# Kernel tuning notes

Measured on AMD Instinct MI355X. Metric: run time of the kernel, lower is better.

The kernel has to match this reference:

```python
import jax, jax.numpy as jnp
import numpy as np

LENA, BATCH, ARR, HID = 8, 128, 1024, 64


def setup_inputs() -> dict:
    key = jax.random.key(0)
    ks = jax.random.split(key, 7)
    s = 0.1  # keep gates out of saturation
    return {
        "x": jax.random.normal(ks[0], (BATCH, ARR, 1), jnp.float32),
        "hn": jnp.zeros((LENA, BATCH, HID), jnp.float32),  # per-LSTM h0 (torch (1,B,H) squeezed)
        "Wih": jax.random.normal(ks[1], (LENA, 4 * HID, 1), jnp.float32) * s,
        "Whh": jax.random.normal(ks[2], (LENA, 4 * HID, HID), jnp.float32) * s,
        "bih": jax.random.normal(ks[3], (LENA, 4 * HID), jnp.float32) * s,
        "bhh": jax.random.normal(ks[4], (LENA, 4 * HID), jnp.float32) * s,
        "Wl": jax.random.normal(ks[5], (LENA, ARR), jnp.float32) * s,
        "bl": jax.random.normal(ks[6], (LENA,), jnp.float32) * s,
    }


def _ensemble_lstm_last_unit(x, hn, Wih, Whh, bias):
    # x: (B, T); hn: (L, B, H). All L LSTMs run fused in one scan over time.
    L, B, H = hn.shape
    c0 = jnp.zeros_like(hn)

    def step(carry, x_t):  # x_t: (B,)
        h, c = carry  # (L, B, H)
        gates = (x_t[None, :, None] * Wih[:, None, :, 0]
                 + jnp.einsum('lbh,lgh->lbg', h, Whh)
                 + bias[:, None, :])  # (L, B, 4H)
        i, f, g, o = jnp.split(gates, 4, axis=-1)  # torch gate order i,f,g,o
        i, f, o = jax.nn.sigmoid(i), jax.nn.sigmoid(f), jax.nn.sigmoid(o)
        c = f * c + i * jnp.tanh(g)
        h = o * jnp.tanh(c)
        return (h, c), h[:, :, -1]  # emit last hidden unit: o[:, :, -1]

    _, ys = jax.lax.scan(step, (hn, c0), x.T)  # ys: (T, L, B)
    return ys


def reference(x, hn, Wih, Whh, bih, bhh, Wl, bl):
    bias = bih + bhh  # (L, 4H)
    ys = _ensemble_lstm_last_unit(x[:, :, 0], hn, Wih, Whh, bias)  # (T, L, B)
    r = ys.sum(axis=1).T  # sum over ensemble -> (B, T=arr_size)
    return r @ Wl.T + bl  # (B, lenA)
```

## Files before the change

kernel.cpp:

```cpp
#include <hip/hip_runtime.h>


#define LENA 8
#define NB 128
#define NT 1024
#define NH 64

typedef __attribute__((ext_vector_type(4))) float f32x4;
typedef __attribute__((ext_vector_type(8))) short bf16x8;

__device__ __forceinline__ short f2bf(float f) {
    unsigned u = __float_as_uint(f);
    unsigned r = (u + 0x7FFFu + ((u >> 16) & 1u)) >> 16;
    return (short)r;
}

__global__ __launch_bounds__(256, 2) void lstm_v16_kernel(
    const float* __restrict__ x, const float* __restrict__ hn,
    const float* __restrict__ Wih, const float* __restrict__ Whh,
    const float* __restrict__ bih, const float* __restrict__ bhh,
    const float* __restrict__ Wl, float* __restrict__ ws)
{
    __shared__ float x2[NT][2];
    __shared__ float ring[NT][2];
    __shared__ __align__(16) short hbuf[2][16][8];
    __shared__ float pws[2][2][8];

    const int tid = threadIdx.x;
    const int w   = tid >> 6;
    const int l   = tid & 63;
    const int col = l & 15;
    const int kg  = l >> 4;
    const int bb  = kg & 1;
    const int li  = blockIdx.x >> 6;
    const int bg  = blockIdx.x & 63;
    const int b0  = bg * 2;

    for (int i = tid; i < 2 * NT; i += 256) {
        int bx = i >> 10, t = i & (NT - 1);
        x2[t][bx] = x[(size_t)(b0 + bx) * NT + t];
    }
    if (tid < 128) {
        int b = tid >> 6, u = tid & 63;
        float v = hn[((size_t)li * NB + b0 + b) * NH + u];
        int slot = b * 8 + ((u >> 3) ^ (2 * b));
        hbuf[0][slot][u & 7] = f2bf(v);
    }

    const float RLN2 = 1.44269504f;
    bf16x8 bf[4][2];
    #pragma unroll
    for (int g = 0; g < 4; ++g) {
        const float sc = (g == 2) ? 2.0f * RLN2 : RLN2;
        const float* rp = Whh + ((size_t)li * 256 + 64 * g + 16 * w + col) * 64 + kg * 8;
        #pragma unroll
        for (int kh = 0; kh < 2; ++kh) {
            const float* q = rp + kh * 32;
            bf16x8 f;
            #pragma unroll
            for (int e = 0; e < 8; ++e) f[e] = f2bf(sc * q[e]);
            bf[g][kh] = f;
        }
    }
    const int u_c = 16 * w + col;
    float wih4[4];
    f32x4 cinit[4];
    #pragma unroll
    for (int g = 0; g < 4; ++g) {
        const float sc = (g == 2) ? 2.0f * RLN2 : RLN2;
        int rowc = li * 256 + 64 * g + u_c;
        wih4[g] = sc * Wih[rowc];
        float bv = sc * (bih[rowc] + bhh[rowc]);
        cinit[g][0] = bv; cinit[g][1] = bv; cinit[g][2] = bv; cinit[g][3] = bv;
    }

    const int b_r = (col >> 2) & 1;
    const int s0 = b_r * 8 + (kg ^ (2 * b_r));
    const int s1 = b_r * 8 + ((4 + kg) ^ (2 * b_r));
    const int wslot = bb * 8 + ((u_c >> 3) ^ (2 * bb));
    const int wpos  = u_c & 7;
    const bool isring = (u_c == 63);

    float cst = 0.0f;

    __syncthreads();

    #pragma unroll 2
    for (int t = 0; t < NT; ++t) {
        const int p = t & 1;
        bf16x8 a0 = *(const bf16x8*)&hbuf[p][s0][0];
        bf16x8 a1 = *(const bf16x8*)&hbuf[p][s1][0];
        const float xv = x2[t][bb];

        f32x4 acc[4];
        __builtin_amdgcn_s_setprio(1);
        #pragma unroll
        for (int g = 0; g < 4; ++g) {
            f32x4 a = __builtin_amdgcn_mfma_f32_16x16x32_bf16(a0, bf[g][0], cinit[g], 0, 0, 0);
            acc[g] = __builtin_amdgcn_mfma_f32_16x16x32_bf16(a1, bf[g][1], a, 0, 0, 0);
        }
        __builtin_amdgcn_s_setprio(0);
        __builtin_amdgcn_sched_barrier(0);

        float gi = fmaf(xv, wih4[0], acc[0][0]);
        float gf = fmaf(xv, wih4[1], acc[1][0]);
        float gg = fmaf(xv, wih4[2], acc[2][0]);
        float go = fmaf(xv, wih4[3], acc[3][0]);

        float iv = __builtin_amdgcn_rcpf(1.0f + __builtin_amdgcn_exp2f(-gi));
        float fv = __builtin_amdgcn_rcpf(1.0f + __builtin_amdgcn_exp2f(-gf));
        float gt = fmaf(-5.77078016f, __builtin_amdgcn_rcpf(1.0f + __builtin_amdgcn_exp2f(gg)), 2.88539008f);
        float ov = __builtin_amdgcn_rcpf(1.0f + __builtin_amdgcn_exp2f(-go));
        cst = fmaf(fv, cst, iv * gt);
        float ct = fmaf(-2.0f, __builtin_amdgcn_rcpf(1.0f + __builtin_amdgcn_exp2f(cst)), 1.0f);
        float hh = ov * ct;

        unsigned pk;
        asm("v_cvt_pk_bf16_f32 %0, %1, %2" : "=v"(pk) : "v"(hh), "v"(hh));
        hbuf[p ^ 1][wslot][wpos] = (short)(pk & 0xffffu);
        if (isring) ring[t][bb] = hh;
        __syncthreads();
    }

    {
        const int b = w >> 1, p2 = w & 1;
        const int a = l & 7, ch = l >> 3;
        const int tb = p2 * 512 + ch * 64;
        const float* wlp = Wl + (size_t)a * NT + tb;
        float pacc = 0.0f;
        #pragma unroll 4
        for (int i = 0; i < 64; ++i)
            pacc = fmaf(ring[tb + i][b], wlp[i], pacc);
        pacc += __shfl_xor(pacc, 8);
        pacc += __shfl_xor(pacc, 16);
        pacc += __shfl_xor(pacc, 32);
        if (l < 8) pws[b][p2][a] = pacc;
    }
    __syncthreads();
    if (tid < 16) {
        int b = tid >> 3, a = tid & 7;
        ws[((size_t)blockIdx.x * 2 + b) * 8 + a] = pws[b][0][a] + pws[b][1][a];
    }
}

__global__ __launch_bounds__(256) void reduce_kernel(
    const float* __restrict__ ws, const float* __restrict__ bl, float* __restrict__ out)
{
    int tid = blockIdx.x * 256 + threadIdx.x;
    if (tid >= NB * LENA) return;
    int b = tid >> 3, a = tid & 7;
    int bg = b >> 1, bx = b & 1;
    float s = bl[a];
    #pragma unroll
    for (int li = 0; li < LENA; ++li)
        s += ws[(((size_t)li * 64 + bg) * 2 + bx) * 8 + a];
    out[tid] = s;
}

extern "C" void kernel_launch(void* const* d_in, const int* in_sizes, int n_in,
                              void* d_out, int out_size, void* d_ws, size_t ws_size,
                              hipStream_t stream) {
    const float* x   = (const float*)d_in[0];
    const float* hn  = (const float*)d_in[1];
    const float* Wih = (const float*)d_in[2];
    const float* Whh = (const float*)d_in[3];
    const float* bih = (const float*)d_in[4];
    const float* bhh = (const float*)d_in[5];
    const float* Wl  = (const float*)d_in[6];
    const float* bl  = (const float*)d_in[7];
    float* out = (float*)d_out;
    float* ws  = (float*)d_ws;

    lstm_v16_kernel<<<dim3(512), dim3(256), 0, stream>>>(x, hn, Wih, Whh, bih, bhh, Wl, ws);
    reduce_kernel<<<dim3(4), dim3(256), 0, stream>>>(ws, bl, out);
}
```

Baseline: 249.9 us.

## Split gate nonlinearities across redundant lane halves using permlane32 swap

The MFMA output is duplicated across lane groups. The change makes lanes kg<2 compute the i/f gates and lanes kg>=2 compute the g/o gates, halving the per-lane transcendental work, and uses permlane32_swap to exchange the g and o values between halves. It negates the sigmoid weight scaling so that exp2 needs no negation. Only the low-half lanes write h to the shared buffer and ring; the others write to a scratch area. The cost is two cross-lane swaps on the serial recurrence path.

```diff
diff --git a/kernel.cpp b/kernel.cpp
--- a/kernel.cpp
+++ b/kernel.cpp
@@ -15,7 +15,7 @@
     return (short)r;
 }
 
-__global__ __launch_bounds__(256, 2) void lstm_v16_kernel(
+__global__ __launch_bounds__(256, 2) void lstm_v18_kernel(
     const float* __restrict__ x, const float* __restrict__ hn,
     const float* __restrict__ Wih, const float* __restrict__ Whh,
     const float* __restrict__ bih, const float* __restrict__ bhh,
@@ -24,6 +24,7 @@
     __shared__ float x2[NT][2];
     __shared__ float ring[NT][2];
     __shared__ __align__(16) short hbuf[2][16][8];
+    __shared__ short scratch[256];
     __shared__ float pws[2][2][8];
 
     const int tid = threadIdx.x;
@@ -32,6 +33,7 @@
     const int col = l & 15;
     const int kg  = l >> 4;
     const int bb  = kg & 1;
+    const bool role = (kg >= 2);
     const int li  = blockIdx.x >> 6;
     const int bg  = blockIdx.x & 63;
     const int b0  = bg * 2;
@@ -51,7 +53,7 @@
     bf16x8 bf[4][2];
     #pragma unroll
     for (int g = 0; g < 4; ++g) {
-        const float sc = (g == 2) ? 2.0f * RLN2 : RLN2;
+        const float sc = (g == 2) ? 2.0f * RLN2 : -RLN2;
         const float* rp = Whh + ((size_t)li * 256 + 64 * g + 16 * w + col) * 64 + kg * 8;
         #pragma unroll
         for (int kh = 0; kh < 2; ++kh) {
@@ -67,19 +69,23 @@
     f32x4 cinit[4];
     #pragma unroll
     for (int g = 0; g < 4; ++g) {
-        const float sc = (g == 2) ? 2.0f * RLN2 : RLN2;
+        const float sc = (g == 2) ? 2.0f * RLN2 : -RLN2;
         int rowc = li * 256 + 64 * g + u_c;
         wih4[g] = sc * Wih[rowc];
         float bv = sc * (bih[rowc] + bhh[rowc]);
         cinit[g][0] = bv; cinit[g][1] = bv; cinit[g][2] = bv; cinit[g][3] = bv;
     }
+    const float wih_a = role ? wih4[2] : wih4[0];
+    const float wih_b = role ? wih4[3] : wih4[1];
 
     const int b_r = (col >> 2) & 1;
     const int s0 = b_r * 8 + (kg ^ (2 * b_r));
     const int s1 = b_r * 8 + ((4 + kg) ^ (2 * b_r));
     const int wslot = bb * 8 + ((u_c >> 3) ^ (2 * bb));
     const int wpos  = u_c & 7;
-    const bool isring = (u_c == 63);
+    short* const wr0 = (kg < 2) ? &hbuf[1][wslot][wpos] : &scratch[tid];
+    short* const wr1 = (kg < 2) ? &hbuf[0][wslot][wpos] : &scratch[tid];
+    const bool isring = (u_c == 63) && (kg < 2);
 
     float cst = 0.0f;
 
@@ -102,22 +108,31 @@
         __builtin_amdgcn_s_setprio(0);
         __builtin_amdgcn_sched_barrier(0);
 
-        float gi = fmaf(xv, wih4[0], acc[0][0]);
-        float gf = fmaf(xv, wih4[1], acc[1][0]);
-        float gg = fmaf(xv, wih4[2], acc[2][0]);
-        float go = fmaf(xv, wih4[3], acc[3][0]);
+        float ga = fmaf(xv, wih_a, role ? acc[2][0] : acc[0][0]);
+        float gb = fmaf(xv, wih_b, role ? acc[3][0] : acc[1][0]);
 
-        float iv = __builtin_amdgcn_rcpf(1.0f + __builtin_amdgcn_exp2f(-gi));
-        float fv = __builtin_amdgcn_rcpf(1.0f + __builtin_amdgcn_exp2f(-gf));
-        float gt = fmaf(-5.77078016f, __builtin_amdgcn_rcpf(1.0f + __builtin_amdgcn_exp2f(gg)), 2.88539008f);
-        float ov = __builtin_amdgcn_rcpf(1.0f + __builtin_amdgcn_exp2f(-go));
-        cst = fmaf(fv, cst, iv * gt);
-        float ct = fmaf(-2.0f, __builtin_amdgcn_rcpf(1.0f + __builtin_amdgcn_exp2f(cst)), 1.0f);
-        float hh = ov * ct;
+        float Ea = __builtin_amdgcn_exp2f(ga);
+        float Eb = __builtin_amdgcn_exp2f(gb);
+        float ra = __builtin_amdgcn_rcpf(1.0f + Ea);
+        float rb = __builtin_amdgcn_rcpf(1.0f + Eb);
+
+        float gtX = fmaf(-5.77078016f, ra, 2.88539008f);
+
+        unsigned gu = __float_as_uint(gtX);
+        auto rg = __builtin_amdgcn_permlane32_swap(gu, gu, false, false);
+        float g2 = __uint_as_float(rg[1]);
+        unsigned ou = __float_as_uint(rb);
+        auto ro = __builtin_amdgcn_permlane32_swap(ou, ou, false, false);
+        float o2 = __uint_as_float(ro[1]);
+
+        cst = fmaf(rb, cst, ra * g2);
+        float Ec = __builtin_amdgcn_exp2f(cst);
+        float ct = fmaf(-2.0f, __builtin_amdgcn_rcpf(1.0f + Ec), 1.0f);
+        float hh = o2 * ct;
 
         unsigned pk;
         asm("v_cvt_pk_bf16_f32 %0, %1, %2" : "=v"(pk) : "v"(hh), "v"(hh));
-        hbuf[p ^ 1][wslot][wpos] = (short)(pk & 0xffffu);
+        *(p ? wr1 : wr0) = (short)pk;
         if (isring) ring[t][bb] = hh;
         __syncthreads();
     }
@@ -171,6 +186,6 @@
     float* out = (float*)d_out;
     float* ws  = (float*)d_ws;
 
-    lstm_v16_kernel<<<dim3(512), dim3(256), 0, stream>>>(x, hn, Wih, Whh, bih, bhh, Wl, ws);
+    lstm_v18_kernel<<<dim3(512), dim3(256), 0, stream>>>(x, hn, Wih, Whh, bih, bhh, Wl, ws);
     reduce_kernel<<<dim3(4), dim3(256), 0, stream>>>(ws, bl, out);
 }
```

New measurement: 242.1 us. 1.03x faster.
